# Performance work log

Hardware: AMD Instinct MI355X
Metric: run time of the kernel (lower is better)

## Reference

```python
import jax, jax.numpy as jnp
import numpy as np

DIM = 1024
NUM_HEADS = 16
HEAD_DIM = DIM // NUM_HEADS
ROPE_BASE = 10000.0


def apply_rope(x, pos):
    """x: [B, H, N, D] float32, pos: [B, N] int -> rotated x (rotate-half convention)."""
    d = x.shape[-1]
    # inv_freq: [D/2]
    inv_freq = 1.0 / (ROPE_BASE ** (jnp.arange(0, d, 2, dtype=jnp.float32) / d))
    # angles: [B, 1, N, D/2]
    ang = pos.astype(jnp.float32)[:, None, :, None] * inv_freq
    cos = jnp.concatenate([jnp.cos(ang), jnp.cos(ang)], axis=-1)
    sin = jnp.concatenate([jnp.sin(ang), jnp.sin(ang)], axis=-1)
    x1, x2 = x[..., : d // 2], x[..., d // 2 :]
    rotated = jnp.concatenate([-x2, x1], axis=-1)
    return x * cos + rotated * sin


def setup_inputs() -> dict:
    key = jax.random.key(0)
    ks = jax.random.split(key, 10)
    B, Nq, Nk, C = 4, 512, 2048, DIM
    scale = 0.02
    inp = {
        "query": jax.random.normal(ks[0], (B, Nq, C), dtype=jnp.float32),
        "key": jax.random.normal(ks[1], (B, Nk, C), dtype=jnp.float32),
        "value": jax.random.normal(ks[2], (B, Nk, C), dtype=jnp.float32),
        "qpos": jnp.sort(jax.random.randint(ks[3], (B, Nq), 0, Nk, dtype=jnp.int32), axis=-1),
        "kpos": jnp.sort(jax.random.randint(ks[4], (B, Nk), 0, Nk, dtype=jnp.int32), axis=-1),
        # learned params (qkv_bias=False; output proj has bias, per nn.Linear default)
        "Wq": jax.random.normal(ks[5], (C, C), dtype=jnp.float32) * scale,
        "Wk": jax.random.normal(ks[6], (C, C), dtype=jnp.float32) * scale,
        "Wv": jax.random.normal(ks[7], (C, C), dtype=jnp.float32) * scale,
        "Wp": jax.random.normal(ks[8], (C, C), dtype=jnp.float32) * scale,
        "bp": jax.random.normal(ks[9], (C,), dtype=jnp.float32) * scale,
    }
    return inp


def reference(query, key, value, qpos, kpos, Wq, Wk, Wv, Wp, bp):
    B, Nq, C = query.shape
    Nk = key.shape[1]
    H, D = NUM_HEADS, C // NUM_HEADS
    scale = D ** (-0.5)

    # separate Q/K/V linear projections (bias=False), split heads -> [B, H, N, D]
    q = (query @ Wq.T).reshape(B, Nq, H, D).transpose(0, 2, 1, 3)
    k = (key @ Wk.T).reshape(B, Nk, H, D).transpose(0, 2, 1, 3)
    v = (value @ Wv.T).reshape(B, Nk, H, D).transpose(0, 2, 1, 3)

    # RoPE applied in fp32 (matches the cast-to-float/rotate/cast-back sequence)
    q = apply_rope(q.astype(jnp.float32), qpos).astype(query.dtype)
    k = apply_rope(k.astype(jnp.float32), kpos).astype(key.dtype)

    # scaled dot-product attention (dropout_p = 0.0, non-causal)
    scores = jnp.einsum("bhqd,bhkd->bhqk", q, k) * scale
    attn = jax.nn.softmax(scores, axis=-1)
    x = jnp.einsum("bhqk,bhkd->bhqd", attn, v)

    # merge heads and output projection (with bias)
    x = x.transpose(0, 2, 1, 3).reshape(B, Nq, C)
    x = x @ Wp.T + bp
    return x
```

## Files before the change

### kernel.cpp

```cpp
#include <hip/hip_runtime.h>
#include <math.h>

#define B_ 4
#define NQ 512
#define NK 2048
#define C_ 1024
#define H_ 16
#define D_ 64
#define KK 1024

typedef __attribute__((ext_vector_type(8))) _Float16 half8;
typedef __attribute__((ext_vector_type(4))) _Float16 half4;
typedef __attribute__((ext_vector_type(4))) float float4v;

__device__ __forceinline__ void g2l16(const _Float16* g, _Float16* l)
{
    __builtin_amdgcn_global_load_lds(
        (const __attribute__((address_space(1))) unsigned int*)g,
        (__attribute__((address_space(3))) unsigned int*)l, 16, 0, 0);
}

__global__ __launch_bounds__(256) void cvt_all(const float* __restrict__ W0,
                                               const float* __restrict__ W1,
                                               const float* __restrict__ W2,
                                               const float* __restrict__ W3,
                                               const float* __restrict__ q,
                                               const float* __restrict__ k,
                                               const float* __restrict__ v,
                                               _Float16* __restrict__ W16,
                                               _Float16* __restrict__ xq,
                                               _Float16* __restrict__ xk,
                                               _Float16* __restrict__ xv,
                                               float2* __restrict__ tab)
{
    const int blk = blockIdx.x;
    if (blk < 256) {
        const int idx = blk * 256 + threadIdx.x;
        const int p = idx >> 5, i = idx & 31;
        double f = 1.0;
        if (i & 1)  f *= 0.7498942093324559;
        if (i & 2)  f *= 0.5623413251903491;
        if (i & 4)  f *= 0.31622776601683794;
        if (i & 8)  f *= 0.1;
        if (i & 16) f *= 0.01;
        const double ang = (double)p * f;
        const double TWO_PI = 6.2831853071795864769;
        const double INV_TWO_PI = 0.15915494309189533577;
        const float red = (float)(ang - TWO_PI * floor(ang * INV_TWO_PI));
        float s, c;
        sincosf(red, &s, &c);
        tab[idx] = make_float2(c, s);
        return;
    }
    const float* src; _Float16* dst; int row;
    if (blk < 4352) {
        const int b1 = blk - 256;
        const int w = b1 >> 10; row = b1 & 1023;
        src = (w == 0) ? W0 : (w == 1) ? W1 : (w == 2) ? W2 : W3;
        dst = W16 + ((size_t)w << 20);
    } else {
        const int b2 = blk - 4352;
        if (b2 < 2048)       { src = q; dst = xq; row = b2; }
        else if (b2 < 10240) { src = k; dst = xk; row = b2 - 2048; }
        else                 { src = v; dst = xv; row = b2 - 10240; }
    }
    const int col = threadIdx.x * 4;
    float4 f = *(const float4*)(src + (size_t)row * 1024 + col);
    half4 h;
    h[0] = (_Float16)f.x; h[1] = (_Float16)f.y;
    h[2] = (_Float16)f.z; h[3] = (_Float16)f.w;
    *(half4*)(dst + (size_t)row * 1024 + col) = h;
}

__device__ __forceinline__ void gemm_body(const _Float16* __restrict__ A,
                                          const _Float16* __restrict__ Bw,
                                          _Float16* __restrict__ Yh,
                                          int mode, int nsh, int m0, int n0,
                                          _Float16* sA, _Float16* sB)
{
    const int tid = threadIdx.x;
    const int lane = tid & 63, wave = tid >> 6;
    const int wm = (wave >> 1) * 64, wn = (wave & 1) * 64;
    const int fm = lane & 15, quad = lane >> 4;

    const int srow = wave * 32 + (lane >> 3);
    const int soct = (lane & 7) ^ (srow & 7);
    const _Float16* gA = A  + (size_t)(m0 + srow) * KK + soct * 8;
    const _Float16* gB = Bw + (size_t)(n0 + srow) * KK + soct * 8;

    float4v acc[4][4];
    #pragma unroll
    for (int i = 0; i < 4; ++i)
        #pragma unroll
        for (int j = 0; j < 4; ++j)
            #pragma unroll
            for (int e = 0; e < 4; ++e) acc[i][j][e] = 0.0f;

    for (int k0 = 0; k0 < KK; k0 += 64) {
        __syncthreads();
        #pragma unroll
        for (int u = 0; u < 4; ++u) {
            g2l16(gA + (size_t)u * 8 * KK + k0, &sA[(wave * 32 + u * 8) * 64]);
            g2l16(gB + (size_t)u * 8 * KK + k0, &sB[(wave * 32 + u * 8) * 64]);
        }
        __syncthreads();

        #pragma unroll
        for (int ks = 0; ks < 2; ++ks) {
            const int po = ((ks * 4 + quad) ^ (fm & 7)) * 8;
            half8 a[4], b[4];
            #pragma unroll
            for (int i = 0; i < 4; ++i) {
                a[i] = *(const half8*)&sA[(wm + i * 16 + fm) * 64 + po];
                b[i] = *(const half8*)&sB[(wn + i * 16 + fm) * 64 + po];
            }
            __builtin_amdgcn_s_setprio(1);
            #pragma unroll
            for (int i = 0; i < 4; ++i)
                #pragma unroll
                for (int j = 0; j < 4; ++j)
                    acc[i][j] = __builtin_amdgcn_mfma_f32_16x16x32_f16(a[i], b[j], acc[i][j], 0, 0, 0);
            __builtin_amdgcn_s_setprio(0);
        }
    }

    const int rr = quad * 4;
    if (mode == 0) {
        const int nmask = (1 << nsh) - 1;
        #pragma unroll
        for (int i = 0; i < 4; ++i)
            #pragma unroll
            for (int r = 0; r < 4; ++r) {
                const int m = m0 + wm + i * 16 + rr + r;
                const int b = m >> nsh, n = m & nmask;
                #pragma unroll
                for (int j = 0; j < 4; ++j) {
                    const int c = n0 + wn + j * 16 + fm;
                    Yh[((((size_t)b * H_ + (c >> 6)) << nsh) + n) * 64 + (c & 63)] = (_Float16)acc[i][j][r];
                }
            }
    } else {
        const int nmask = (1 << nsh) - 1;
        #pragma unroll
        for (int i = 0; i < 4; ++i)
            #pragma unroll
            for (int r = 0; r < 4; ++r) {
                const int m = m0 + wm + i * 16 + rr + r;
                const int b = m >> nsh, n = m & nmask;
                #pragma unroll
                for (int j = 0; j < 4; ++j) {
                    const int c = n0 + wn + j * 16 + fm;
                    Yh[(((size_t)(b * H_ + (c >> 6)) * 64) + (c & 63)) * NK + n] = (_Float16)acc[i][j][r];
                }
            }
    }
}

__global__ __launch_bounds__(256) void gemm_qkv(const _Float16* __restrict__ xq,
                                                const _Float16* __restrict__ xk,
                                                const _Float16* __restrict__ xv,
                                                const _Float16* __restrict__ W16,
                                                _Float16* __restrict__ qhp,
                                                _Float16* __restrict__ khp,
                                                _Float16* __restrict__ vtp)
{
    __shared__ _Float16 sA[128 * 64];
    __shared__ _Float16 sB[128 * 64];

    const int lbid = blockIdx.x;
    const int xcd = lbid & 7;
    const int seq = lbid >> 3;
    const int y = xcd + 8 * (seq >> 3);
    const int n0 = (seq & 7) * 128;

    if (y < 64)
        gemm_body(xk, W16 + (1u << 20), khp, 0, 11, y * 128, n0, sA, sB);
    else if (y < 128)
        gemm_body(xv, W16 + (2u << 20), vtp, 2, 11, (y - 64) * 128, n0, sA, sB);
    else
        gemm_body(xq, W16, qhp, 0, 9, (y - 128) * 128, n0, sA, sB);
}

__global__ __launch_bounds__(256) void gemm_out(const _Float16* __restrict__ A,
                                                const _Float16* __restrict__ Bw,
                                                float* __restrict__ Yf,
                                                const float* __restrict__ bias)
{
    __shared__ _Float16 sA[64 * 64];
    __shared__ _Float16 sB[128 * 64];

    const int tid = threadIdx.x;
    const int lane = tid & 63, wave = tid >> 6;
    const int n0 = blockIdx.x * 128, m0 = blockIdx.y * 64;
    const int wm = (wave >> 1) * 32, wn = (wave & 1) * 64;
    const int fm = lane & 15, quad = lane >> 4;

    const int r0 = lane >> 3;
    const int srowA = wave * 16 + r0;
    const int srowB = wave * 32 + r0;
    const _Float16* gA = A  + (size_t)(m0 + srowA) * KK + (((lane & 7) ^ r0) * 8);
    const _Float16* gB = Bw + (size_t)(n0 + srowB) * KK + (((lane & 7) ^ r0) * 8);

    float4v acc[2][4];
    #pragma unroll
    for (int i = 0; i < 2; ++i)
        #pragma unroll
        for (int j = 0; j < 4; ++j)
            #pragma unroll
            for (int e = 0; e < 4; ++e) acc[i][j][e] = 0.0f;

    for (int k0 = 0; k0 < KK; k0 += 64) {
        __syncthreads();
        #pragma unroll
        for (int u = 0; u < 2; ++u)
            g2l16(gA + (size_t)u * 8 * KK + k0, &sA[(wave * 16 + u * 8) * 64]);
        #pragma unroll
        for (int u = 0; u < 4; ++u)
            g2l16(gB + (size_t)u * 8 * KK + k0, &sB[(wave * 32 + u * 8) * 64]);
        __syncthreads();

        #pragma unroll
        for (int ks = 0; ks < 2; ++ks) {
            const int po = ((ks * 4 + quad) ^ (fm & 7)) * 8;
            half8 a[2], b[4];
            #pragma unroll
            for (int i = 0; i < 2; ++i)
                a[i] = *(const half8*)&sA[(wm + i * 16 + fm) * 64 + po];
            #pragma unroll
            for (int j = 0; j < 4; ++j)
                b[j] = *(const half8*)&sB[(wn + j * 16 + fm) * 64 + po];
            __builtin_amdgcn_s_setprio(1);
            #pragma unroll
            for (int i = 0; i < 2; ++i)
                #pragma unroll
                for (int j = 0; j < 4; ++j)
                    acc[i][j] = __builtin_amdgcn_mfma_f32_16x16x32_f16(a[i], b[j], acc[i][j], 0, 0, 0);
            __builtin_amdgcn_s_setprio(0);
        }
    }

    const int rr = quad * 4;
    #pragma unroll
    for (int i = 0; i < 2; ++i)
        #pragma unroll
        for (int r = 0; r < 4; ++r) {
            const int m = m0 + wm + i * 16 + rr + r;
            #pragma unroll
            for (int j = 0; j < 4; ++j) {
                const int c = n0 + wn + j * 16 + fm;
                Yf[(size_t)m * 1024 + c] = acc[i][j][r] + bias[c];
            }
        }
}

__global__ __launch_bounds__(256) void rope_tab(_Float16* __restrict__ qh,
                                                _Float16* __restrict__ kh,
                                                const int* __restrict__ qpos,
                                                const int* __restrict__ kpos,
                                                const float2* __restrict__ tab)
{
    const int idx = blockIdx.x * 256 + threadIdx.x;
    const int row = idx >> 3;
    const int d0 = (idx & 7) * 4;

    _Float16* ptr; int p; float scale;
    if (row < 32768) {
        ptr = qh + (size_t)row * 64;
        p = qpos[(row >> 13) * 512 + (row & 511)];
        scale = 0.125f;
    } else {
        const int rk = row - 32768;
        ptr = kh + (size_t)rk * 64;
        p = kpos[(rk >> 15) * 2048 + (rk & 2047)];
        scale = 1.0f;
    }

    half4 x1 = *(const half4*)(ptr + d0);
    half4 x2 = *(const half4*)(ptr + d0 + 32);
    const float2* tb = tab + p * 32 + d0;
    half4 o1, o2;
    #pragma unroll
    for (int u = 0; u < 4; ++u) {
        const float2 cs = tb[u];
        const float a = (float)x1[u], b = (float)x2[u];
        o1[u] = (_Float16)((a * cs.x - b * cs.y) * scale);
        o2[u] = (_Float16)((b * cs.x + a * cs.y) * scale);
    }
    *(half4*)(ptr + d0)      = o1;
    *(half4*)(ptr + d0 + 32) = o2;
}

__global__ __launch_bounds__(256) void attn_fused(const _Float16* __restrict__ qh,
                                                  const _Float16* __restrict__ kh,
                                                  const _Float16* __restrict__ vt,
                                                  _Float16* __restrict__ xw16)
{
    __shared__ _Float16 sK[3][64 * 64];
    __shared__ _Float16 sV[3][64 * 64];
    __shared__ _Float16 ps[4][16][66];

    const int tid = threadIdx.x;
    const int lane = tid & 63, wv = tid >> 6;
    const int bhi = blockIdx.x & 63;
    const int qoct = blockIdx.x >> 6;
    const size_t bh = (size_t)bhi;
    const int qt = qoct * 4 + wv;

    const int fm = lane & 15;
    const int quad = lane >> 4;
    const int fq = quad * 8;

    const _Float16* kb = kh + bh * NK * 64;
    const _Float16* vb = vt + bh * (size_t)64 * NK;

    const int r0 = lane >> 3;
    const int c4 = lane & 7;
    const int sch = c4 ^ r0;
    const _Float16* gK = kb + (size_t)(wv * 16 + r0) * 64 + sch * 8;
    const _Float16* gV = vb + (size_t)(wv * 16 + r0) * NK + sch * 8;

#define STAGE(bf, t) do {                                                     \
        g2l16(gK + (size_t)(t) * 4096,        &sK[bf][(wv * 16) * 64]);       \
        g2l16(gK + (size_t)(t) * 4096 + 512,  &sK[bf][(wv * 16 + 8) * 64]);   \
        g2l16(gV + (t) * 64,                  &sV[bf][(wv * 16) * 64]);       \
        g2l16(gV + (size_t)8 * NK + (t) * 64, &sV[bf][(wv * 16 + 8) * 64]);   \
    } while (0)

    const _Float16* qb = qh + (bh * NQ + (size_t)qt * 16) * 64;
    half8 aq[2];
    aq[0] = *(const half8*)(qb + (size_t)fm * 64 + fq);
    aq[1] = *(const half8*)(qb + (size_t)fm * 64 + 32 + fq);

    float l_acc[4] = {};
    float4v O[4];
    #pragma unroll
    for (int j = 0; j < 4; ++j)
        #pragma unroll
        for (int e = 0; e < 4; ++e) O[j][e] = 0.0f;

    const float4v z4 = {0.0f, 0.0f, 0.0f, 0.0f};

    STAGE(0, 0);
    STAGE(1, 1);

    for (int it = 0; it < 32; ++it) {
        const int cur = it % 3;

        if (it < 31) asm volatile("s_waitcnt vmcnt(4)" ::: "memory");
        else         asm volatile("s_waitcnt vmcnt(0)" ::: "memory");
        __builtin_amdgcn_sched_barrier(0);
        __builtin_amdgcn_s_barrier();
        __builtin_amdgcn_sched_barrier(0);

        if (it + 2 < 32)
            STAGE((it + 2) % 3, it + 2);

        const _Float16* Kc = sK[cur];
        const _Float16* Vc = sV[cur];

        half8 bk[4][2];
        #pragma unroll
        for (int j = 0; j < 4; ++j)
            #pragma unroll
            for (int ks = 0; ks < 2; ++ks)
                bk[j][ks] = *(const half8*)&Kc[(j * 16 + fm) * 64 + (((ks * 4 + quad) ^ (fm & 7)) * 8)];

        float4v s[4];
        __builtin_amdgcn_s_setprio(1);
        #pragma unroll
        for (int j = 0; j < 4; ++j) {
            s[j] = __builtin_amdgcn_mfma_f32_16x16x32_f16(aq[0], bk[j][0], z4, 0, 0, 0);
            s[j] = __builtin_amdgcn_mfma_f32_16x16x32_f16(aq[1], bk[j][1], s[j], 0, 0, 0);
        }
        __builtin_amdgcn_s_setprio(0);

        half8 bv[4][2];
        #pragma unroll
        for (int j = 0; j < 4; ++j)
            #pragma unroll
            for (int ks = 0; ks < 2; ++ks)
                bv[j][ks] = *(const half8*)&Vc[(j * 16 + fm) * 64 + (((ks * 4 + quad) ^ (fm & 7)) * 8)];

        #pragma unroll
        for (int j = 0; j < 4; ++j)
            #pragma unroll
            for (int r = 0; r < 4; ++r) {
                const float p = __expf(s[j][r]);
                l_acc[r] += p;
                ps[wv][quad * 4 + r][16 * j + fm] = (_Float16)p;
            }

        __builtin_amdgcn_s_setprio(1);
        #pragma unroll
        for (int ks = 0; ks < 2; ++ks) {
            half8 pa = *(const half8*)&ps[wv][fm][ks * 32 + fq];
            #pragma unroll
            for (int j = 0; j < 4; ++j)
                O[j] = __builtin_amdgcn_mfma_f32_16x16x32_f16(pa, bv[j][ks], O[j], 0, 0, 0);
        }
        __builtin_amdgcn_s_setprio(0);
    }
#undef STAGE

    #pragma unroll
    for (int r = 0; r < 4; ++r) {
        float l = l_acc[r];
        l += __shfl_xor(l, 1);
        l += __shfl_xor(l, 2);
        l += __shfl_xor(l, 4);
        l += __shfl_xor(l, 8);
        const float inv = 1.0f / l;
        const int qr = quad * 4 + r;
        const int row = (bhi >> 4) * 512 + qt * 16 + qr;
        #pragma unroll
        for (int j = 0; j < 4; ++j) {
            const int col = (bhi & 15) * 64 + j * 16 + fm;
            xw16[(size_t)row * 1024 + col] = (_Float16)(O[j][r] * inv);
        }
    }
}

extern "C" void kernel_launch(void* const* d_in, const int* in_sizes, int n_in,
                              void* d_out, int out_size, void* d_ws, size_t ws_size,
                              hipStream_t stream)
{
    const float* query = (const float*)d_in[0];
    const float* key   = (const float*)d_in[1];
    const float* value = (const float*)d_in[2];
    const int*   qpos  = (const int*)d_in[3];
    const int*   kpos  = (const int*)d_in[4];
    const float* Wq    = (const float*)d_in[5];
    const float* Wk    = (const float*)d_in[6];
    const float* Wv    = (const float*)d_in[7];
    const float* Wp    = (const float*)d_in[8];
    const float* bp    = (const float*)d_in[9];
    float* out = (float*)d_out;

    char* ws = (char*)d_ws;
    _Float16* xk16  = (_Float16*)(ws);
    _Float16* xv16  = (_Float16*)(ws + (16u << 20));
    _Float16* xq16  = (_Float16*)(ws + (32u << 20));
    _Float16* W16   = (_Float16*)(ws + (36u << 20));
    _Float16* qhp   = (_Float16*)(ws + (44u << 20));
    _Float16* khp   = (_Float16*)(ws + (48u << 20));
    _Float16* vtp   = (_Float16*)(ws + (64u << 20));
    float2*   tab   = (float2*)d_out;

    cvt_all<<<22784, 256, 0, stream>>>(Wq, Wk, Wv, Wp, query, key, value,
                                       W16, xq16, xk16, xv16, tab);

    gemm_qkv<<<1152, 256, 0, stream>>>(xq16, xk16, xv16, W16, qhp, khp, vtp);

    rope_tab<<<5120, 256, 0, stream>>>(qhp, khp, qpos, kpos, tab);

    attn_fused<<<512, 256, 0, stream>>>(qhp, khp, vtp, xq16);

    gemm_out<<<dim3(8, 32), 256, 0, stream>>>(xq16, W16 + (3u << 20), out, bp);
}
```

Before: 248.7 us.

## Split attention key tiles across two wave groups with LDS reduction

Doubles the attention block to 512 threads (8 waves). Each pair of waves handles the same 16 query rows, and each wave processes half of every 64-key tile. Partial O and row sums are then combined through LDS at the end. The intent is more waves in flight per CU, to hide latency and spread the exp/MFMA work across more wavefronts. In exchange it adds an end-of-kernel reduction with two extra barriers and reuses the K/V LDS as a scratch buffer, and with only 512 blocks occupancy may be limited by register use.

```diff
diff --git a/kernel.cpp b/kernel.cpp
--- a/kernel.cpp
+++ b/kernel.cpp
@@ -290,21 +290,23 @@
     *(half4*)(ptr + d0 + 32) = o2;
 }
 
-__global__ __launch_bounds__(256) void attn_fused(const _Float16* __restrict__ qh,
+__global__ __launch_bounds__(512) void attn_fused(const _Float16* __restrict__ qh,
                                                   const _Float16* __restrict__ kh,
                                                   const _Float16* __restrict__ vt,
                                                   _Float16* __restrict__ xw16)
 {
     __shared__ _Float16 sK[3][64 * 64];
     __shared__ _Float16 sV[3][64 * 64];
-    __shared__ _Float16 ps[4][16][66];
+    __shared__ _Float16 ps2[8][16][34];
 
     const int tid = threadIdx.x;
-    const int lane = tid & 63, wv = tid >> 6;
+    const int lane = tid & 63, w = tid >> 6;
+    const int qt4 = w & 3;
+    const int kh2 = w >> 2;
     const int bhi = blockIdx.x & 63;
     const int qoct = blockIdx.x >> 6;
     const size_t bh = (size_t)bhi;
-    const int qt = qoct * 4 + wv;
+    const int qt = qoct * 4 + qt4;
 
     const int fm = lane & 15;
     const int quad = lane >> 4;
@@ -316,14 +318,12 @@
     const int r0 = lane >> 3;
     const int c4 = lane & 7;
     const int sch = c4 ^ r0;
-    const _Float16* gK = kb + (size_t)(wv * 16 + r0) * 64 + sch * 8;
-    const _Float16* gV = vb + (size_t)(wv * 16 + r0) * NK + sch * 8;
-
-#define STAGE(bf, t) do {                                                     \
-        g2l16(gK + (size_t)(t) * 4096,        &sK[bf][(wv * 16) * 64]);       \
-        g2l16(gK + (size_t)(t) * 4096 + 512,  &sK[bf][(wv * 16 + 8) * 64]);   \
-        g2l16(gV + (t) * 64,                  &sV[bf][(wv * 16) * 64]);       \
-        g2l16(gV + (size_t)8 * NK + (t) * 64, &sV[bf][(wv * 16 + 8) * 64]);   \
+    const _Float16* gK = kb + (size_t)(w * 8 + r0) * 64 + sch * 8;
+    const _Float16* gV = vb + (size_t)(w * 8 + r0) * NK + sch * 8;
+
+#define STAGE(bf, t) do {                                             \
+        g2l16(gK + (size_t)(t) * 4096, &sK[bf][(w * 8) * 64]);        \
+        g2l16(gV + (t) * 64,           &sV[bf][(w * 8) * 64]);        \
     } while (0)
 
     const _Float16* qb = qh + (bh * NQ + (size_t)qt * 16) * 64;
@@ -346,7 +346,7 @@
     for (int it = 0; it < 32; ++it) {
         const int cur = it % 3;
 
-        if (it < 31) asm volatile("s_waitcnt vmcnt(4)" ::: "memory");
+        if (it < 31) asm volatile("s_waitcnt vmcnt(2)" ::: "memory");
         else         asm volatile("s_waitcnt vmcnt(0)" ::: "memory");
         __builtin_amdgcn_sched_barrier(0);
         __builtin_amdgcn_s_barrier();
@@ -358,50 +358,48 @@
         const _Float16* Kc = sK[cur];
         const _Float16* Vc = sV[cur];
 
-        half8 bk[4][2];
+        half8 bk[2][2];
+        #pragma unroll
+        for (int jl = 0; jl < 2; ++jl)
+            #pragma unroll
+            for (int ks = 0; ks < 2; ++ks)
+                bk[jl][ks] = *(const half8*)&Kc[((kh2 * 2 + jl) * 16 + fm) * 64 + (((ks * 4 + quad) ^ (fm & 7)) * 8)];
+
+        float4v s[2];
+        __builtin_amdgcn_s_setprio(1);
+        #pragma unroll
+        for (int jl = 0; jl < 2; ++jl) {
+            s[jl] = __builtin_amdgcn_mfma_f32_16x16x32_f16(aq[0], bk[jl][0], z4, 0, 0, 0);
+            s[jl] = __builtin_amdgcn_mfma_f32_16x16x32_f16(aq[1], bk[jl][1], s[jl], 0, 0, 0);
+        }
+        __builtin_amdgcn_s_setprio(0);
+
+        half8 bv[4];
         #pragma unroll
         for (int j = 0; j < 4; ++j)
-            #pragma unroll
-            for (int ks = 0; ks < 2; ++ks)
-                bk[j][ks] = *(const half8*)&Kc[(j * 16 + fm) * 64 + (((ks * 4 + quad) ^ (fm & 7)) * 8)];
-
-        float4v s[4];
+            bv[j] = *(const half8*)&Vc[(j * 16 + fm) * 64 + (((kh2 * 4 + quad) ^ (fm & 7)) * 8)];
+
+        #pragma unroll
+        for (int jl = 0; jl < 2; ++jl)
+            #pragma unroll
+            for (int r = 0; r < 4; ++r) {
+                const float p = __expf(s[jl][r]);
+                l_acc[r] += p;
+                ps2[w][quad * 4 + r][16 * jl + fm] = (_Float16)p;
+            }
+
         __builtin_amdgcn_s_setprio(1);
-        #pragma unroll
-        for (int j = 0; j < 4; ++j) {
-            s[j] = __builtin_amdgcn_mfma_f32_16x16x32_f16(aq[0], bk[j][0], z4, 0, 0, 0);
-            s[j] = __builtin_amdgcn_mfma_f32_16x16x32_f16(aq[1], bk[j][1], s[j], 0, 0, 0);
+        {
+            half8 pa = *(const half8*)&ps2[w][fm][fq];
+            #pragma unroll
+            for (int j = 0; j < 4; ++j)
+                O[j] = __builtin_amdgcn_mfma_f32_16x16x32_f16(pa, bv[j], O[j], 0, 0, 0);
         }
         __builtin_amdgcn_s_setprio(0);
-
-        half8 bv[4][2];
-        #pragma unroll
-        for (int j = 0; j < 4; ++j)
-            #pragma unroll
-            for (int ks = 0; ks < 2; ++ks)
-                bv[j][ks] = *(const half8*)&Vc[(j * 16 + fm) * 64 + (((ks * 4 + quad) ^ (fm & 7)) * 8)];
-
-        #pragma unroll
-        for (int j = 0; j < 4; ++j)
-            #pragma unroll
-            for (int r = 0; r < 4; ++r) {
-                const float p = __expf(s[j][r]);
-                l_acc[r] += p;
-                ps[wv][quad * 4 + r][16 * j + fm] = (_Float16)p;
-            }
-
-        __builtin_amdgcn_s_setprio(1);
-        #pragma unroll
-        for (int ks = 0; ks < 2; ++ks) {
-            half8 pa = *(const half8*)&ps[wv][fm][ks * 32 + fq];
-            #pragma unroll
-            for (int j = 0; j < 4; ++j)
-                O[j] = __builtin_amdgcn_mfma_f32_16x16x32_f16(pa, bv[j][ks], O[j], 0, 0, 0);
-        }
-        __builtin_amdgcn_s_setprio(0);
     }
 #undef STAGE
 
+    float lr[4];
     #pragma unroll
     for (int r = 0; r < 4; ++r) {
         float l = l_acc[r];
@@ -409,13 +407,35 @@
         l += __shfl_xor(l, 2);
         l += __shfl_xor(l, 4);
         l += __shfl_xor(l, 8);
-        const float inv = 1.0f / l;
-        const int qr = quad * 4 + r;
-        const int row = (bhi >> 4) * 512 + qt * 16 + qr;
-        #pragma unroll
-        for (int j = 0; j < 4; ++j) {
-            const int col = (bhi & 15) * 64 + j * 16 + fm;
-            xw16[(size_t)row * 1024 + col] = (_Float16)(O[j][r] * inv);
+        lr[r] = l;
+    }
+
+    __syncthreads();
+
+    float* cb = (float*)sK;
+    float* lb = (float*)sV;
+    if (kh2 == 1) {
+        #pragma unroll
+        for (int r = 0; r < 4; ++r) {
+            const int qr = quad * 4 + r;
+            #pragma unroll
+            for (int j = 0; j < 4; ++j)
+                cb[qt4 * 1024 + qr * 64 + j * 16 + fm] = O[j][r];
+            if (fm == 0) lb[qt4 * 16 + qr] = lr[r];
+        }
+    }
+    __syncthreads();
+    if (kh2 == 0) {
+        #pragma unroll
+        for (int r = 0; r < 4; ++r) {
+            const int qr = quad * 4 + r;
+            const float inv = 1.0f / (lr[r] + lb[qt4 * 16 + qr]);
+            const int row = (bhi >> 4) * 512 + qt * 16 + qr;
+            #pragma unroll
+            for (int j = 0; j < 4; ++j) {
+                const float o = O[j][r] + cb[qt4 * 1024 + qr * 64 + j * 16 + fm];
+                xw16[(size_t)row * 1024 + (bhi & 15) * 64 + j * 16 + fm] = (_Float16)(o * inv);
+            }
         }
     }
 }
@@ -453,7 +473,7 @@
 
     rope_tab<<<5120, 256, 0, stream>>>(qhp, khp, qpos, kpos, tab);
 
-    attn_fused<<<512, 256, 0, stream>>>(qhp, khp, vtp, xq16);
+    attn_fused<<<512, 512, 0, stream>>>(qhp, khp, vtp, xq16);
 
     gemm_out<<<dim3(8, 32), 256, 0, stream>>>(xq16, W16 + (3u << 20), out, bp);
 }
```

Result: faster. 237.9 us (-4.4%).
